# Performance work log

Measured on AMD Instinct MI355X. Metric: run time of the kernel, lower is better.

## Reference

```python
import jax, jax.numpy as jnp
import numpy as np

B, N, C_IN, C_OUT, K = 2, 8192, 128, 128, 21  # K = num_neighbors + 1 (self)
EPS = 1e-5

def knn_idx(xyz, k):
    # xyz: [B,N,3] -> idx [B,N,k] of k nearest neighbors (self included)
    d2 = jnp.sum(xyz * xyz, axis=-1)  # [B,N]
    dist = d2[:, :, None] + d2[:, None, :] - 2.0 * jnp.einsum('bnd,bmd->bnm', xyz, xyz)
    _, idx = jax.lax.top_k(-dist, k)
    return idx

def group_points(pts, idx):
    # pts [B,N,D], idx [B,N,K] -> [B,N,K,D]
    return jax.vmap(lambda p, i: p[i])(pts, idx)

def group_feats(f, idx):
    # f [B,C,N], idx [B,N,K] -> [B,C,N,K]
    return jax.vmap(lambda ff, i: ff[:, i])(f, idx)

def conv_bn_relu(x, W, g, b, m, v):
    # 1x1 conv (bias=False) + BatchNorm (inference stats) + ReLU
    y = jnp.einsum('oc,bcnk->bonk', W, x)
    inv = g / jnp.sqrt(v + EPS)
    return jax.nn.relu(y * inv[None, :, None, None] + (b - m * inv)[None, :, None, None])

def setup_inputs():
    key = jax.random.key(0)
    ks = jax.random.split(key, 12)
    return {
        'xyz': jax.random.normal(ks[0], (B, N, 3), jnp.float32),
        'f': jax.random.normal(ks[1], (B, C_IN, N), jnp.float32),
        'W_geo': jax.random.normal(ks[2], (C_OUT, 6), jnp.float32) * 0.1,
        'g_geo': jax.random.uniform(ks[3], (C_OUT,), jnp.float32, 0.5, 1.5),
        'b_geo': jax.random.normal(ks[4], (C_OUT,), jnp.float32) * 0.1,
        'm_geo': jax.random.normal(ks[5], (C_OUT,), jnp.float32) * 0.1,
        'v_geo': jax.random.uniform(ks[6], (C_OUT,), jnp.float32, 0.5, 1.5),
        'W_feat': jax.random.normal(ks[7], (C_OUT, 2 * C_IN), jnp.float32) * 0.05,
        'g_feat': jax.random.uniform(ks[8], (C_OUT,), jnp.float32, 0.5, 1.5),
        'b_feat': jax.random.normal(ks[9], (C_OUT,), jnp.float32) * 0.1,
        'm_feat': jax.random.normal(ks[10], (C_OUT,), jnp.float32) * 0.1,
        'v_feat': jax.random.uniform(ks[11], (C_OUT,), jnp.float32, 0.5, 1.5),
    }

def reference(xyz, f, W_geo, g_geo, b_geo, m_geo, v_geo, W_feat, g_feat, b_feat, m_feat, v_feat):
    idx = knn_idx(xyz, K)                                   # [B,N,K]
    grouped_xyz = group_points(xyz, idx)                    # [B,N,K,3]
    xyz_diff = jnp.transpose(grouped_xyz - xyz[:, :, None, :], (0, 3, 1, 2))  # [B,3,N,K]
    center = jnp.broadcast_to(jnp.transpose(xyz, (0, 2, 1))[:, :, :, None], (B, 3, N, K))
    G_geo = jnp.concatenate([center, xyz_diff], axis=1)     # [B,6,N,K]
    grouped_f = group_feats(f, idx)                         # [B,C,N,K]
    center_f = jnp.broadcast_to(f[:, :, :, None], (B, C_IN, N, K))
    G_feat = jnp.concatenate([center_f, grouped_f - center_f], axis=1)  # [B,2C,N,K]
    G_geo = conv_bn_relu(G_geo, W_geo, g_geo, b_geo, m_geo, v_geo)      # [B,C_OUT,N,K]
    G_feat = conv_bn_relu(G_feat, W_feat, g_feat, b_feat, m_feat, v_feat)
    feature = jnp.concatenate([G_geo, G_feat], axis=1)      # [B,2*C_OUT,N,K]
    return jnp.max(feature, axis=-1)                        # [B,2*C_OUT,N]
```

## Files before the change

kernel.cpp:

```cpp
#include <hip/hip_runtime.h>

typedef unsigned int u32;
typedef unsigned long long u64;
typedef unsigned short u16;

#define DEV __device__ __forceinline__

DEV u16 f2bf(float x) {
  u32 u = __float_as_uint(x);
  u32 r = u + 0x7fffu + ((u >> 16) & 1u);
  return (u16)(r >> 16);
}
DEV float bflo(u32 d) { return __uint_as_float(d << 16); }
DEV float bfhi(u32 d) { return __uint_as_float(d & 0xffff0000u); }
DEV u64 sortable64(double f) {
  long long b = __double_as_longlong(f);
  return (u64)b ^ (u64)((b >> 63) | (long long)0x8000000000000000ll);
}
DEV double ddist(double qx, double qy, double qz, double qd2,
                 float mxf, float myf, float mzf) {
  double cx = (double)mxf, cy = (double)myf, cz = (double)mzf;
  double cd2 = cx * cx + cy * cy + cz * cz;
  double dot = cx * qx + cy * qy + cz * qz;
  return (qd2 + cd2) - 2.0 * dot;
}

#define NB 2
#define NN 8192
#define NC 128
#define KK 21
#define MARGIN 1e-3f

__global__ __launch_bounds__(1024) void k_knnprep(
    const float* __restrict__ xyz, int* __restrict__ knn,
    const float* __restrict__ Wf, const float* __restrict__ gf, const float* __restrict__ bf_,
    const float* __restrict__ mf, const float* __restrict__ vf,
    const float* __restrict__ Wg, const float* __restrict__ gg, const float* __restrict__ bg,
    const float* __restrict__ mg, const float* __restrict__ vg,
    u16* __restrict__ Wt, float* __restrict__ beta_f,
    float* __restrict__ Wgu, float* __restrict__ Wgv, float* __restrict__ beta_g) {
  __shared__ float4 sc[NN];
  __shared__ u16 ssurv[64][128];
  __shared__ u32 scnt[64];

  const int t = threadIdx.x;

  if (blockIdx.x < 32) {
    int g = (blockIdx.x << 10) + t;
    int c = g >> 8, o = g & 255;
    float val;
    if (o < 128) {
      float inv = gf[o] / sqrtf(vf[o] + 1e-5f);
      val = inv * (Wf[o * 256 + c] - Wf[o * 256 + c + 128]);
    } else {
      int o2 = o - 128;
      float inv = gf[o2] / sqrtf(vf[o2] + 1e-5f);
      val = inv * Wf[o2 * 256 + c + 128];
    }
    Wt[c * 256 + o] = f2bf(val);
    if (g < 128) {
      float inv = gf[g] / sqrtf(vf[g] + 1e-5f);
      beta_f[g] = bf_[g] - mf[g] * inv;
    } else if (g < 256) {
      int oo = g - 128;
      float invg = gg[oo] / sqrtf(vg[oo] + 1e-5f);
#pragma unroll
      for (int d = 0; d < 3; ++d) {
        Wgu[oo * 3 + d] = invg * (Wg[oo * 6 + d] - Wg[oo * 6 + 3 + d]);
        Wgv[oo * 3 + d] = invg * Wg[oo * 6 + 3 + d];
      }
      beta_g[oo] = bg[oo] - mg[oo] * invg;
    }
    return;
  }

  const int kb = blockIdx.x - 32;
  const int b = kb >> 7;
  const int n0 = (kb & 127) << 6;
  const float* X = xyz + b * (NN * 3);

  if (t < 64) scnt[t] = 0u;

  const int w = t >> 6, lane = t & 63;

  float mx[4], my[4], mz[4];
#pragma unroll
  for (int i = 0; i < 4; ++i) {
    int q = n0 + (w << 2) + i;
    mx[i] = -2.0f * X[q * 3];
    my[i] = -2.0f * X[q * 3 + 1];
    mz[i] = -2.0f * X[q * 3 + 2];
  }

#pragma unroll
  for (int k = 0; k < 8; ++k) {
    int c = (k << 10) + t;
    float x = X[c * 3], y = X[c * 3 + 1], z = X[c * 3 + 2];
    float d2 = __builtin_fmaf(x, x, __builtin_fmaf(y, y, z * z));
    sc[c] = make_float4(x, y, z, d2);
  }
  __syncthreads();

  float mn[4];
#pragma unroll
  for (int i = 0; i < 4; ++i) mn[i] = __builtin_inff();

#pragma unroll 4
  for (int cc = 0; cc < NN; cc += 64) {
    float4 C = sc[cc + lane];
#pragma unroll
    for (int i = 0; i < 4; ++i) {
      float s = __builtin_fmaf(C.x, mx[i],
                __builtin_fmaf(C.y, my[i],
                __builtin_fmaf(C.z, mz[i], C.w)));
      mn[i] = fminf(mn[i], s);
    }
  }

  float thr[4];
#pragma unroll
  for (int i = 0; i < 4; ++i) {
    float v = mn[i];
#pragma unroll
    for (int k = 2; k <= 64; k <<= 1) {
#pragma unroll
      for (int j = k >> 1; j > 0; j >>= 1) {
        float p = __shfl_xor(v, j);
        bool takeMin = (((lane & k) == 0) == ((lane & j) == 0));
        v = takeMin ? fminf(v, p) : fmaxf(v, p);
      }
    }
    thr[i] = __shfl(v, 20) + MARGIN;
  }

#pragma unroll 2
  for (int cc = 0; cc < NN; cc += 64) {
    float4 C = sc[cc + lane];
    int mbase = cc + lane;
#pragma unroll
    for (int i = 0; i < 4; ++i) {
      float s = __builtin_fmaf(C.x, mx[i],
                __builtin_fmaf(C.y, my[i],
                __builtin_fmaf(C.z, mz[i], C.w)));
      if (s <= thr[i]) {
        int qq = (w << 2) + i;
        u32 slot = atomicAdd(&scnt[qq], 1u);
        if (slot < 128u) ssurv[qq][slot] = (u16)mbase;
      }
    }
  }
  __syncthreads();

#pragma unroll 1
  for (int i = 0; i < 4; ++i) {
    const int qq = (w << 2) + i;
    const int q = n0 + qq;
    double Qx = (double)X[q * 3], Qy = (double)X[q * 3 + 1], Qz = (double)X[q * 3 + 2];
    double Qd2 = Qx * Qx + Qy * Qy + Qz * Qz;
    u32 cnt = scnt[qq];
    int* outp = knn + ((b << 13) + q) * KK;

    bool v0 = ((u32)lane < cnt);
    u32 m0 = v0 ? (u32)ssurv[qq][lane] : 0u;
    double s0 = ddist(Qx, Qy, Qz, Qd2, X[m0 * 3], X[m0 * 3 + 1], X[m0 * 3 + 2]);
    u64 k0 = v0 ? ((sortable64(s0) & 0xFFFFFFFFFFFFE000ull) | (u64)m0) : ~0ull;

    if (cnt <= 64u) {
      u64 v = k0;
#pragma unroll
      for (int k = 2; k <= 64; k <<= 1) {
#pragma unroll
        for (int j = k >> 1; j > 0; j >>= 1) {
          u64 p = __shfl_xor(v, j);
          bool takeMin = (((lane & k) == 0) == ((lane & j) == 0));
          bool pl = p < v;
          u64 mnv = pl ? p : v;
          u64 mxv = pl ? v : p;
          v = takeMin ? mnv : mxv;
        }
      }
      if (lane < KK) outp[lane] = (int)(v & 8191ull);
    } else {
      bool v1 = ((u32)(lane + 64) < cnt);
      u32 m1 = v1 ? (u32)ssurv[qq][lane + 64] : 0u;
      double s1 = ddist(Qx, Qy, Qz, Qd2, X[m1 * 3], X[m1 * 3 + 1], X[m1 * 3 + 2]);
      u64 k1 = v1 ? ((sortable64(s1) & 0xFFFFFFFFFFFFE000ull) | (u64)m1) : ~0ull;
      u32 selm = 0;
      for (int r = 0; r < KK; ++r) {
        u64 mk = (k0 < k1) ? k0 : k1;
#pragma unroll
        for (int j = 32; j > 0; j >>= 1) {
          u64 p = __shfl_xor(mk, j);
          if (p < mk) mk = p;
        }
        if (k0 == mk) k0 = ~0ull;
        else if (k1 == mk) k1 = ~0ull;
        if (lane == r) selm = (u32)(mk & 8191ull);
      }
      if (lane < KK) outp[lane] = (int)selm;
    }
  }
}

__global__ __launch_bounds__(256) void k_featgeo(
    const float* __restrict__ f, const u32* __restrict__ Wt32, const float* __restrict__ beta_f,
    const float* __restrict__ xyz, const float* __restrict__ Wgu, const float* __restrict__ Wgv,
    const float* __restrict__ beta_g, u32* __restrict__ ucat, u32* __restrict__ vcat) {
  __shared__ u32 sW[128 * 64];
  __shared__ float sF[128][68];

  const int t = threadIdx.x;

  if (blockIdx.x >= 512) {
    int g = ((blockIdx.x - 512) << 8) + t;
    int p = g >> 6, oc = g & 63;
    const float* xp = xyz + p * 3;
    float X = xp[0], Y = xp[1], Z = xp[2];
    u32 du = 0, dv = 0;
#pragma unroll
    for (int h = 0; h < 2; ++h) {
      int o = oc * 2 + h;
      float ug = X * Wgu[o * 3] + Y * Wgu[o * 3 + 1] + Z * Wgu[o * 3 + 2] + beta_g[o];
      float vv = X * Wgv[o * 3] + Y * Wgv[o * 3 + 1] + Z * Wgv[o * 3 + 2];
      du |= (u32)f2bf(ug) << (16 * h);
      dv |= (u32)f2bf(vv) << (16 * h);
    }
    ucat[p * 128 + oc] = du;
    vcat[p * 128 + oc] = dv;
    return;
  }

  const int blk = blockIdx.x;
  const int H = blk & 1;
  const int b = blk >> 8;
  const int n0 = ((blk >> 1) & 127) << 6;
  const int boff = b * (NC * NN);

#pragma unroll
  for (int k = 0; k < 32; ++k) {
    int i = t + (k << 8);
    sW[i] = Wt32[((i >> 6) << 7) + (H << 6) + (i & 63)];
  }
#pragma unroll
  for (int k = 0; k < 32; ++k) {
    int i = t + (k << 8);
    int c = i >> 6, col = i & 63;
    sF[c][col] = f[boff + c * NN + n0 + col];
  }
  __syncthreads();

  const int w = t >> 6, lane = t & 63;
  const int og = lane >> 4, pg = lane & 15;
  const int o0 = (w << 5) + (og << 3);
  const int p0 = pg << 2;

  float acc[8][4];
#pragma unroll
  for (int a = 0; a < 8; ++a)
#pragma unroll
    for (int p = 0; p < 4; ++p) acc[a][p] = 0.0f;

  for (int c = 0; c < 128; ++c) {
    float4 fa = *(const float4*)&sF[c][p0];
    uint4 wr = *(const uint4*)&sW[(c << 6) + (o0 >> 1)];
    float wv[8] = {bflo(wr.x), bfhi(wr.x), bflo(wr.y), bfhi(wr.y),
                   bflo(wr.z), bfhi(wr.z), bflo(wr.w), bfhi(wr.w)};
    float fv[4] = {fa.x, fa.y, fa.z, fa.w};
#pragma unroll
    for (int a = 0; a < 8; ++a)
#pragma unroll
      for (int p = 0; p < 4; ++p) acc[a][p] = __builtin_fmaf(wv[a], fv[p], acc[a][p]);
  }

  float bet[8];
#pragma unroll
  for (int a = 0; a < 8; ++a) bet[a] = (H == 0) ? beta_f[o0 + a] : 0.0f;
  u32* dstbase = (H == 0) ? ucat : vcat;
#pragma unroll
  for (int p = 0; p < 4; ++p) {
    int pt = (b << 13) + n0 + p0 + p;
    u32 d0 = (u32)f2bf(acc[0][p] + bet[0]) | ((u32)f2bf(acc[1][p] + bet[1]) << 16);
    u32 d1 = (u32)f2bf(acc[2][p] + bet[2]) | ((u32)f2bf(acc[3][p] + bet[3]) << 16);
    u32 d2 = (u32)f2bf(acc[4][p] + bet[4]) | ((u32)f2bf(acc[5][p] + bet[5]) << 16);
    u32 d3 = (u32)f2bf(acc[6][p] + bet[6]) | ((u32)f2bf(acc[7][p] + bet[7]) << 16);
    *(uint4*)&dstbase[pt * 128 + 64 + (o0 >> 1)] = make_uint4(d0, d1, d2, d3);
  }
}

__global__ __launch_bounds__(256) void k_gather(
    const u32* __restrict__ ucat, const u32* __restrict__ vcat,
    const int* __restrict__ knn, float* __restrict__ out) {
  __shared__ float tr[64 * 65];

  const int t = threadIdx.x;
  const int blk = blockIdx.x;
  const int Q = blk & 3;
  const int b = blk >> 9;
  const int n0 = ((blk >> 2) & 127) << 6;
  const int w = t >> 6, lane = t & 63;
  const int half = lane >> 5;
  const int l32 = lane & 31;
  const int lo = (Q << 5) | l32;

  for (int step = 0; step < 8; ++step) {
    int qq = (step << 3) + (w << 1) + half;
    int q = n0 + qq;
    const int* ip = knn + ((b << 13) + q) * KK;
    float a0 = -__builtin_inff(), a1 = -__builtin_inff();
#pragma unroll
    for (int k = 0; k < KK; ++k) {
      int p = ip[k];
      u32 d = vcat[(((b << 13) + p) << 7) + lo];
      a0 = fmaxf(a0, bflo(d));
      a1 = fmaxf(a1, bfhi(d));
    }
    u32 u = ucat[(((b << 13) + q) << 7) + lo];
    tr[qq * 65 + l32] = fmaxf(bflo(u) + a0, 0.0f);
    tr[qq * 65 + 32 + l32] = fmaxf(bfhi(u) + a1, 0.0f);
  }
  __syncthreads();

  float* ob = out + b * (256 * NN) + (Q << 6) * NN;
  for (int i = 0; i < 16; ++i) {
    int o = (w << 4) + i;
    int col = ((o & 1) << 5) + (o >> 1);
    ob[o * NN + n0 + lane] = tr[lane * 65 + col];
  }
}

extern "C" void kernel_launch(void* const* d_in, const int* in_sizes, int n_in,
                              void* d_out, int out_size, void* d_ws, size_t ws_size,
                              hipStream_t stream) {
  const float* xyz = (const float*)d_in[0];
  const float* f   = (const float*)d_in[1];
  const float* Wg  = (const float*)d_in[2];
  const float* gg  = (const float*)d_in[3];
  const float* bg  = (const float*)d_in[4];
  const float* mg  = (const float*)d_in[5];
  const float* vg  = (const float*)d_in[6];
  const float* Wf  = (const float*)d_in[7];
  const float* gf  = (const float*)d_in[8];
  const float* bf_ = (const float*)d_in[9];
  const float* mf  = (const float*)d_in[10];
  const float* vf  = (const float*)d_in[11];

  char* ws = (char*)d_ws;
  u16*   Wt     = (u16*)ws;
  float* beta_f = (float*)(ws + 65536);
  float* Wgu    = (float*)(ws + 66048);
  float* Wgv    = (float*)(ws + 67584);
  float* beta_g = (float*)(ws + 69120);
  u32*   ucat   = (u32*)(ws + 69632);
  u32*   vcat   = (u32*)(ws + 69632 + 8388608);
  int*   knn    = (int*)(ws + 69632 + 2 * 8388608);
  float* out    = (float*)d_out;

  if (ws_size < (size_t)(69632 + 2 * 8388608 + 16384 * KK * 4)) return;

  k_knnprep<<<dim3(288), dim3(1024), 0, stream>>>(
      xyz, knn, Wf, gf, bf_, mf, vf, Wg, gg, bg, mg, vg,
      Wt, beta_f, Wgu, Wgv, beta_g);
  k_featgeo<<<dim3(4608), dim3(256), 0, stream>>>(
      f, (const u32*)Wt, beta_f, xyz, Wgu, Wgv, beta_g, ucat, vcat);
  k_gather<<<dim3(1024), dim3(256), 0, stream>>>(ucat, vcat, knn, out);
}
```

Baseline: 175.3 us.

## Merge kNN and feature/geo projection into one kernel, fold BN weights per block

Combines the kNN kernel and the feature/geometry projection kernel into a single launch. The first 256 blocks do kNN and the other 256 blocks each handle a 64-point tile across all 256 output columns with 1024 threads. Each projection block recomputes the BN-folded bf16 weights and the geometry weights itself instead of reading them from a prep pass. This removes one launch and the weight-prep dependency, and lets the kNN and projection work overlap. In exchange, every block repeats the weight folding with many scattered global reads of Wf, and the larger shared-memory footprint may lower occupancy.

```diff
diff --git a/kernel.cpp b/kernel.cpp
--- a/kernel.cpp
+++ b/kernel.cpp
@@ -24,6 +24,17 @@
   double dot = cx * qx + cy * qy + cz * qz;
   return (qd2 + cd2) - 2.0 * dot;
 }
+DEV float foldW(const float* __restrict__ Wf, const float* __restrict__ gf,
+                const float* __restrict__ vf, int o, int c) {
+  if (o < 128) {
+    float inv = gf[o] / sqrtf(vf[o] + 1e-5f);
+    return inv * (Wf[o * 256 + c] - Wf[o * 256 + c + 128]);
+  } else {
+    int o2 = o - 128;
+    float inv = gf[o2] / sqrtf(vf[o2] + 1e-5f);
+    return inv * Wf[o2 * 256 + c + 128];
+  }
+}
 
 #define NB 2
 #define NN 8192
@@ -31,259 +42,260 @@
 #define KK 21
 #define MARGIN 1e-3f
 
-__global__ __launch_bounds__(1024) void k_knnprep(
+__global__ __launch_bounds__(1024) void k_mega(
     const float* __restrict__ xyz, int* __restrict__ knn,
+    const float* __restrict__ f,
     const float* __restrict__ Wf, const float* __restrict__ gf, const float* __restrict__ bf_,
     const float* __restrict__ mf, const float* __restrict__ vf,
     const float* __restrict__ Wg, const float* __restrict__ gg, const float* __restrict__ bg,
     const float* __restrict__ mg, const float* __restrict__ vg,
-    u16* __restrict__ Wt, float* __restrict__ beta_f,
-    float* __restrict__ Wgu, float* __restrict__ Wgv, float* __restrict__ beta_g) {
-  __shared__ float4 sc[NN];
-  __shared__ u16 ssurv[64][128];
-  __shared__ u32 scnt[64];
-
+    u32* __restrict__ ucat, u32* __restrict__ vcat) {
+  __shared__ alignas(16) char smem[147712];
   const int t = threadIdx.x;
 
-  if (blockIdx.x < 32) {
-    int g = (blockIdx.x << 10) + t;
-    int c = g >> 8, o = g & 255;
-    float val;
-    if (o < 128) {
-      float inv = gf[o] / sqrtf(vf[o] + 1e-5f);
-      val = inv * (Wf[o * 256 + c] - Wf[o * 256 + c + 128]);
-    } else {
-      int o2 = o - 128;
-      float inv = gf[o2] / sqrtf(vf[o2] + 1e-5f);
-      val = inv * Wf[o2 * 256 + c + 128];
-    }
-    Wt[c * 256 + o] = f2bf(val);
-    if (g < 128) {
-      float inv = gf[g] / sqrtf(vf[g] + 1e-5f);
-      beta_f[g] = bf_[g] - mf[g] * inv;
-    } else if (g < 256) {
-      int oo = g - 128;
-      float invg = gg[oo] / sqrtf(vg[oo] + 1e-5f);
-#pragma unroll
-      for (int d = 0; d < 3; ++d) {
-        Wgu[oo * 3 + d] = invg * (Wg[oo * 6 + d] - Wg[oo * 6 + 3 + d]);
-        Wgv[oo * 3 + d] = invg * Wg[oo * 6 + 3 + d];
-      }
-      beta_g[oo] = bg[oo] - mg[oo] * invg;
+  if (blockIdx.x < 256) {
+    float4* sc = (float4*)smem;
+    u16 (*ssurv)[128] = (u16(*)[128])(smem + 131072);
+    u32* scnt = (u32*)(smem + 131072 + 16384);
+
+    const int kb = blockIdx.x;
+    const int b = kb >> 7;
+    const int n0 = (kb & 127) << 6;
+    const float* X = xyz + b * (NN * 3);
+
+    if (t < 64) scnt[t] = 0u;
+
+    const int w = t >> 6, lane = t & 63;
+
+    float mx[4], my[4], mz[4];
+#pragma unroll
+    for (int i = 0; i < 4; ++i) {
+      int q = n0 + (w << 2) + i;
+      mx[i] = -2.0f * X[q * 3];
+      my[i] = -2.0f * X[q * 3 + 1];
+      mz[i] = -2.0f * X[q * 3 + 2];
+    }
+
+#pragma unroll
+    for (int k = 0; k < 8; ++k) {
+      int c = (k << 10) + t;
+      float x = X[c * 3], y = X[c * 3 + 1], z = X[c * 3 + 2];
+      float d2 = __builtin_fmaf(x, x, __builtin_fmaf(y, y, z * z));
+      sc[c] = make_float4(x, y, z, d2);
+    }
+    __syncthreads();
+
+    float mn[4];
+#pragma unroll
+    for (int i = 0; i < 4; ++i) mn[i] = __builtin_inff();
+
+#pragma unroll 4
+    for (int cc = 0; cc < NN; cc += 64) {
+      float4 C = sc[cc + lane];
+#pragma unroll
+      for (int i = 0; i < 4; ++i) {
+        float s = __builtin_fmaf(C.x, mx[i],
+                  __builtin_fmaf(C.y, my[i],
+                  __builtin_fmaf(C.z, mz[i], C.w)));
+        mn[i] = fminf(mn[i], s);
+      }
+    }
+
+    float thr[4];
+#pragma unroll
+    for (int i = 0; i < 4; ++i) {
+      float v = mn[i];
+#pragma unroll
+      for (int k = 2; k <= 64; k <<= 1) {
+#pragma unroll
+        for (int j = k >> 1; j > 0; j >>= 1) {
+          float p = __shfl_xor(v, j);
+          bool takeMin = (((lane & k) == 0) == ((lane & j) == 0));
+          v = takeMin ? fminf(v, p) : fmaxf(v, p);
+        }
+      }
+      thr[i] = __shfl(v, 20) + MARGIN;
+    }
+
+#pragma unroll 2
+    for (int cc = 0; cc < NN; cc += 64) {
+      float4 C = sc[cc + lane];
+      int mbase = cc + lane;
+#pragma unroll
+      for (int i = 0; i < 4; ++i) {
+        float s = __builtin_fmaf(C.x, mx[i],
+                  __builtin_fmaf(C.y, my[i],
+                  __builtin_fmaf(C.z, mz[i], C.w)));
+        if (s <= thr[i]) {
+          int qq = (w << 2) + i;
+          u32 slot = atomicAdd(&scnt[qq], 1u);
+          if (slot < 128u) ssurv[qq][slot] = (u16)mbase;
+        }
+      }
+    }
+    __syncthreads();
+
+#pragma unroll 1
+    for (int i = 0; i < 4; ++i) {
+      const int qq = (w << 2) + i;
+      const int q = n0 + qq;
+      double Qx = (double)X[q * 3], Qy = (double)X[q * 3 + 1], Qz = (double)X[q * 3 + 2];
+      double Qd2 = Qx * Qx + Qy * Qy + Qz * Qz;
+      u32 cnt = scnt[qq];
+      int* outp = knn + ((b << 13) + q) * KK;
+
+      bool v0 = ((u32)lane < cnt);
+      u32 m0 = v0 ? (u32)ssurv[qq][lane] : 0u;
+      double s0 = ddist(Qx, Qy, Qz, Qd2, X[m0 * 3], X[m0 * 3 + 1], X[m0 * 3 + 2]);
+      u64 k0 = v0 ? ((sortable64(s0) & 0xFFFFFFFFFFFFE000ull) | (u64)m0) : ~0ull;
+
+      if (cnt <= 64u) {
+        u64 v = k0;
+#pragma unroll
+        for (int k = 2; k <= 64; k <<= 1) {
+#pragma unroll
+          for (int j = k >> 1; j > 0; j >>= 1) {
+            u64 p = __shfl_xor(v, j);
+            bool takeMin = (((lane & k) == 0) == ((lane & j) == 0));
+            bool pl = p < v;
+            u64 mnv = pl ? p : v;
+            u64 mxv = pl ? v : p;
+            v = takeMin ? mnv : mxv;
+          }
+        }
+        if (lane < KK) outp[lane] = (int)(v & 8191ull);
+      } else {
+        bool v1 = ((u32)(lane + 64) < cnt);
+        u32 m1 = v1 ? (u32)ssurv[qq][lane + 64] : 0u;
+        double s1 = ddist(Qx, Qy, Qz, Qd2, X[m1 * 3], X[m1 * 3 + 1], X[m1 * 3 + 2]);
+        u64 k1 = v1 ? ((sortable64(s1) & 0xFFFFFFFFFFFFE000ull) | (u64)m1) : ~0ull;
+        u32 selm = 0;
+        for (int r = 0; r < KK; ++r) {
+          u64 mk = (k0 < k1) ? k0 : k1;
+#pragma unroll
+          for (int j = 32; j > 0; j >>= 1) {
+            u64 p = __shfl_xor(mk, j);
+            if (p < mk) mk = p;
+          }
+          if (k0 == mk) k0 = ~0ull;
+          else if (k1 == mk) k1 = ~0ull;
+          if (lane == r) selm = (u32)(mk & 8191ull);
+        }
+        if (lane < KK) outp[lane] = (int)selm;
+      }
     }
     return;
   }
 
-  const int kb = blockIdx.x - 32;
-  const int b = kb >> 7;
-  const int n0 = (kb & 127) << 6;
-  const float* X = xyz + b * (NN * 3);
-
-  if (t < 64) scnt[t] = 0u;
-
-  const int w = t >> 6, lane = t & 63;
-
-  float mx[4], my[4], mz[4];
-#pragma unroll
-  for (int i = 0; i < 4; ++i) {
-    int q = n0 + (w << 2) + i;
-    mx[i] = -2.0f * X[q * 3];
-    my[i] = -2.0f * X[q * 3 + 1];
-    mz[i] = -2.0f * X[q * 3 + 2];
-  }
-
+  const int fb = blockIdx.x - 256;
+  const int b = fb >> 7;
+  const int n0 = (fb & 127) << 6;
+  const int boff = b * (NC * NN);
+
+  u32* sW = (u32*)smem;
+  float (*sF)[68] = (float(*)[68])(smem + 65536);
+
+#pragma unroll
+  for (int k = 0; k < 16; ++k) {
+    int i = t + (k << 10);
+    int c = i >> 7, j = i & 127;
+    sW[i] = (u32)f2bf(foldW(Wf, gf, vf, 2 * j, c)) |
+            ((u32)f2bf(foldW(Wf, gf, vf, 2 * j + 1, c)) << 16);
+  }
 #pragma unroll
   for (int k = 0; k < 8; ++k) {
-    int c = (k << 10) + t;
-    float x = X[c * 3], y = X[c * 3 + 1], z = X[c * 3 + 2];
-    float d2 = __builtin_fmaf(x, x, __builtin_fmaf(y, y, z * z));
-    sc[c] = make_float4(x, y, z, d2);
-  }
-  __syncthreads();
-
-  float mn[4];
-#pragma unroll
-  for (int i = 0; i < 4; ++i) mn[i] = __builtin_inff();
-
-#pragma unroll 4
-  for (int cc = 0; cc < NN; cc += 64) {
-    float4 C = sc[cc + lane];
-#pragma unroll
-    for (int i = 0; i < 4; ++i) {
-      float s = __builtin_fmaf(C.x, mx[i],
-                __builtin_fmaf(C.y, my[i],
-                __builtin_fmaf(C.z, mz[i], C.w)));
-      mn[i] = fminf(mn[i], s);
-    }
-  }
-
-  float thr[4];
-#pragma unroll
-  for (int i = 0; i < 4; ++i) {
-    float v = mn[i];
-#pragma unroll
-    for (int k = 2; k <= 64; k <<= 1) {
-#pragma unroll
-      for (int j = k >> 1; j > 0; j >>= 1) {
-        float p = __shfl_xor(v, j);
-        bool takeMin = (((lane & k) == 0) == ((lane & j) == 0));
-        v = takeMin ? fminf(v, p) : fmaxf(v, p);
-      }
-    }
-    thr[i] = __shfl(v, 20) + MARGIN;
-  }
-
-#pragma unroll 2
-  for (int cc = 0; cc < NN; cc += 64) {
-    float4 C = sc[cc + lane];
-    int mbase = cc + lane;
-#pragma unroll
-    for (int i = 0; i < 4; ++i) {
-      float s = __builtin_fmaf(C.x, mx[i],
-                __builtin_fmaf(C.y, my[i],
-                __builtin_fmaf(C.z, mz[i], C.w)));
-      if (s <= thr[i]) {
-        int qq = (w << 2) + i;
-        u32 slot = atomicAdd(&scnt[qq], 1u);
-        if (slot < 128u) ssurv[qq][slot] = (u16)mbase;
-      }
-    }
-  }
-  __syncthreads();
-
-#pragma unroll 1
-  for (int i = 0; i < 4; ++i) {
-    const int qq = (w << 2) + i;
-    const int q = n0 + qq;
-    double Qx = (double)X[q * 3], Qy = (double)X[q * 3 + 1], Qz = (double)X[q * 3 + 2];
-    double Qd2 = Qx * Qx + Qy * Qy + Qz * Qz;
-    u32 cnt = scnt[qq];
-    int* outp = knn + ((b << 13) + q) * KK;
-
-    bool v0 = ((u32)lane < cnt);
-    u32 m0 = v0 ? (u32)ssurv[qq][lane] : 0u;
-    double s0 = ddist(Qx, Qy, Qz, Qd2, X[m0 * 3], X[m0 * 3 + 1], X[m0 * 3 + 2]);
-    u64 k0 = v0 ? ((sortable64(s0) & 0xFFFFFFFFFFFFE000ull) | (u64)m0) : ~0ull;
-
-    if (cnt <= 64u) {
-      u64 v = k0;
-#pragma unroll
-      for (int k = 2; k <= 64; k <<= 1) {
-#pragma unroll
-        for (int j = k >> 1; j > 0; j >>= 1) {
-          u64 p = __shfl_xor(v, j);
-          bool takeMin = (((lane & k) == 0) == ((lane & j) == 0));
-          bool pl = p < v;
-          u64 mnv = pl ? p : v;
-          u64 mxv = pl ? v : p;
-          v = takeMin ? mnv : mxv;
-        }
-      }
-      if (lane < KK) outp[lane] = (int)(v & 8191ull);
-    } else {
-      bool v1 = ((u32)(lane + 64) < cnt);
-      u32 m1 = v1 ? (u32)ssurv[qq][lane + 64] : 0u;
-      double s1 = ddist(Qx, Qy, Qz, Qd2, X[m1 * 3], X[m1 * 3 + 1], X[m1 * 3 + 2]);
-      u64 k1 = v1 ? ((sortable64(s1) & 0xFFFFFFFFFFFFE000ull) | (u64)m1) : ~0ull;
-      u32 selm = 0;
-      for (int r = 0; r < KK; ++r) {
-        u64 mk = (k0 < k1) ? k0 : k1;
-#pragma unroll
-        for (int j = 32; j > 0; j >>= 1) {
-          u64 p = __shfl_xor(mk, j);
-          if (p < mk) mk = p;
-        }
-        if (k0 == mk) k0 = ~0ull;
-        else if (k1 == mk) k1 = ~0ull;
-        if (lane == r) selm = (u32)(mk & 8191ull);
-      }
-      if (lane < KK) outp[lane] = (int)selm;
-    }
-  }
-}
-
-__global__ __launch_bounds__(256) void k_featgeo(
-    const float* __restrict__ f, const u32* __restrict__ Wt32, const float* __restrict__ beta_f,
-    const float* __restrict__ xyz, const float* __restrict__ Wgu, const float* __restrict__ Wgv,
-    const float* __restrict__ beta_g, u32* __restrict__ ucat, u32* __restrict__ vcat) {
-  __shared__ u32 sW[128 * 64];
-  __shared__ float sF[128][68];
-
-  const int t = threadIdx.x;
-
-  if (blockIdx.x >= 512) {
-    int g = ((blockIdx.x - 512) << 8) + t;
-    int p = g >> 6, oc = g & 63;
-    const float* xp = xyz + p * 3;
-    float X = xp[0], Y = xp[1], Z = xp[2];
-    u32 du = 0, dv = 0;
-#pragma unroll
-    for (int h = 0; h < 2; ++h) {
-      int o = oc * 2 + h;
-      float ug = X * Wgu[o * 3] + Y * Wgu[o * 3 + 1] + Z * Wgu[o * 3 + 2] + beta_g[o];
-      float vv = X * Wgv[o * 3] + Y * Wgv[o * 3 + 1] + Z * Wgv[o * 3 + 2];
-      du |= (u32)f2bf(ug) << (16 * h);
-      dv |= (u32)f2bf(vv) << (16 * h);
-    }
-    ucat[p * 128 + oc] = du;
-    vcat[p * 128 + oc] = dv;
-    return;
-  }
-
-  const int blk = blockIdx.x;
-  const int H = blk & 1;
-  const int b = blk >> 8;
-  const int n0 = ((blk >> 1) & 127) << 6;
-  const int boff = b * (NC * NN);
-
-#pragma unroll
-  for (int k = 0; k < 32; ++k) {
-    int i = t + (k << 8);
-    sW[i] = Wt32[((i >> 6) << 7) + (H << 6) + (i & 63)];
-  }
-#pragma unroll
-  for (int k = 0; k < 32; ++k) {
-    int i = t + (k << 8);
-    int c = i >> 6, col = i & 63;
-    sF[c][col] = f[boff + c * NN + n0 + col];
+    int i = t + (k << 10);
+    int c = i >> 6, coll = i & 63;
+    sF[c][coll] = f[boff + c * NN + n0 + coll];
   }
   __syncthreads();
 
   const int w = t >> 6, lane = t & 63;
   const int og = lane >> 4, pg = lane & 15;
-  const int o0 = (w << 5) + (og << 3);
+  const int col0 = (w << 3) + (og << 1);
   const int p0 = pg << 2;
 
-  float acc[8][4];
-#pragma unroll
-  for (int a = 0; a < 8; ++a)
+  float acc[4][4];
+#pragma unroll
+  for (int a = 0; a < 4; ++a)
 #pragma unroll
     for (int p = 0; p < 4; ++p) acc[a][p] = 0.0f;
 
   for (int c = 0; c < 128; ++c) {
     float4 fa = *(const float4*)&sF[c][p0];
-    uint4 wr = *(const uint4*)&sW[(c << 6) + (o0 >> 1)];
-    float wv[8] = {bflo(wr.x), bfhi(wr.x), bflo(wr.y), bfhi(wr.y),
-                   bflo(wr.z), bfhi(wr.z), bflo(wr.w), bfhi(wr.w)};
+    uint2 wr = *(const uint2*)&sW[(c << 7) + col0];
+    float wv[4] = {bflo(wr.x), bfhi(wr.x), bflo(wr.y), bfhi(wr.y)};
     float fv[4] = {fa.x, fa.y, fa.z, fa.w};
 #pragma unroll
-    for (int a = 0; a < 8; ++a)
+    for (int a = 0; a < 4; ++a)
 #pragma unroll
       for (int p = 0; p < 4; ++p) acc[a][p] = __builtin_fmaf(wv[a], fv[p], acc[a][p]);
   }
 
-  float bet[8];
-#pragma unroll
-  for (int a = 0; a < 8; ++a) bet[a] = (H == 0) ? beta_f[o0 + a] : 0.0f;
-  u32* dstbase = (H == 0) ? ucat : vcat;
+  const bool isu = (col0 < 64);
+  const int jloc = col0 & 63;
+  float bet[4];
+#pragma unroll
+  for (int a = 0; a < 4; ++a) {
+    if (isu) {
+      int o = 2 * col0 + a;
+      float inv = gf[o] / sqrtf(vf[o] + 1e-5f);
+      bet[a] = bf_[o] - mf[o] * inv;
+    } else bet[a] = 0.0f;
+  }
+  u32* dstbase = isu ? ucat : vcat;
 #pragma unroll
   for (int p = 0; p < 4; ++p) {
     int pt = (b << 13) + n0 + p0 + p;
     u32 d0 = (u32)f2bf(acc[0][p] + bet[0]) | ((u32)f2bf(acc[1][p] + bet[1]) << 16);
     u32 d1 = (u32)f2bf(acc[2][p] + bet[2]) | ((u32)f2bf(acc[3][p] + bet[3]) << 16);
-    u32 d2 = (u32)f2bf(acc[4][p] + bet[4]) | ((u32)f2bf(acc[5][p] + bet[5]) << 16);
-    u32 d3 = (u32)f2bf(acc[6][p] + bet[6]) | ((u32)f2bf(acc[7][p] + bet[7]) << 16);
-    *(uint4*)&dstbase[pt * 128 + 64 + (o0 >> 1)] = make_uint4(d0, d1, d2, d3);
+    *(uint2*)&dstbase[pt * 128 + 64 + jloc] = make_uint2(d0, d1);
+  }
+
+  {
+    const int side = t >> 9;
+    const int tl = t & 511;
+    const int oc = tl & 63;
+    const int pr = tl >> 6;
+    float w0x, w0y, w0z, b0, w1x, w1y, w1z, b1;
+    {
+      int o = oc * 2;
+      float invg = gg[o] / sqrtf(vg[o] + 1e-5f);
+      if (side == 0) {
+        w0x = invg * (Wg[o * 6] - Wg[o * 6 + 3]);
+        w0y = invg * (Wg[o * 6 + 1] - Wg[o * 6 + 4]);
+        w0z = invg * (Wg[o * 6 + 2] - Wg[o * 6 + 5]);
+        b0 = bg[o] - mg[o] * invg;
+      } else {
+        w0x = invg * Wg[o * 6 + 3];
+        w0y = invg * Wg[o * 6 + 4];
+        w0z = invg * Wg[o * 6 + 5];
+        b0 = 0.0f;
+      }
+      int o1 = o + 1;
+      float invg1 = gg[o1] / sqrtf(vg[o1] + 1e-5f);
+      if (side == 0) {
+        w1x = invg1 * (Wg[o1 * 6] - Wg[o1 * 6 + 3]);
+        w1y = invg1 * (Wg[o1 * 6 + 1] - Wg[o1 * 6 + 4]);
+        w1z = invg1 * (Wg[o1 * 6 + 2] - Wg[o1 * 6 + 5]);
+        b1 = bg[o1] - mg[o1] * invg1;
+      } else {
+        w1x = invg1 * Wg[o1 * 6 + 3];
+        w1y = invg1 * Wg[o1 * 6 + 4];
+        w1z = invg1 * Wg[o1 * 6 + 5];
+        b1 = 0.0f;
+      }
+    }
+    u32* dst = (side == 0) ? ucat : vcat;
+#pragma unroll
+    for (int jj = 0; jj < 8; ++jj) {
+      int p = n0 + pr + (jj << 3);
+      const float* xp = xyz + ((b << 13) + p) * 3;
+      float X = xp[0], Y = xp[1], Z = xp[2];
+      float v0 = X * w0x + Y * w0y + Z * w0z + b0;
+      float v1 = X * w1x + Y * w1y + Z * w1z + b1;
+      dst[(((b << 13) + p) << 7) + oc] = (u32)f2bf(v0) | ((u32)f2bf(v1) << 16);
+    }
   }
 }
 
@@ -345,11 +357,6 @@
   const float* vf  = (const float*)d_in[11];
 
   char* ws = (char*)d_ws;
-  u16*   Wt     = (u16*)ws;
-  float* beta_f = (float*)(ws + 65536);
-  float* Wgu    = (float*)(ws + 66048);
-  float* Wgv    = (float*)(ws + 67584);
-  float* beta_g = (float*)(ws + 69120);
   u32*   ucat   = (u32*)(ws + 69632);
   u32*   vcat   = (u32*)(ws + 69632 + 8388608);
   int*   knn    = (int*)(ws + 69632 + 2 * 8388608);
@@ -357,10 +364,7 @@
 
   if (ws_size < (size_t)(69632 + 2 * 8388608 + 16384 * KK * 4)) return;
 
-  k_knnprep<<<dim3(288), dim3(1024), 0, stream>>>(
-      xyz, knn, Wf, gf, bf_, mf, vf, Wg, gg, bg, mg, vg,
-      Wt, beta_f, Wgu, Wgv, beta_g);
-  k_featgeo<<<dim3(4608), dim3(256), 0, stream>>>(
-      f, (const u32*)Wt, beta_f, xyz, Wgu, Wgv, beta_g, ucat, vcat);
+  k_mega<<<dim3(512), dim3(1024), 0, stream>>>(
+      xyz, knn, f, Wf, gf, bf_, mf, vf, Wg, gg, bg, mg, vg, ucat, vcat);
   k_gather<<<dim3(1024), dim3(256), 0, stream>>>(ucat, vcat, knn, out);
 }
```

Measured after the change: 203.6 us. 1.16x slower.
